# Optimization experiments

Hardware: AMD Instinct MI355X
Metric: run time of the kernel (lower is better)

## Reference

```python
import jax, jax.numpy as jnp
import numpy as np

B, Hdim, Wdim, C, HEADS, WS = 16, 112, 112, 128, 4, 7
VD = C
MLP_H = int(4.0 * VD)
EPS = 1e-5


def _layernorm(x, g, b):
    mu = jnp.mean(x, axis=-1, keepdims=True)
    var = jnp.mean(jnp.square(x - mu), axis=-1, keepdims=True)
    return (x - mu) * jax.lax.rsqrt(var + EPS) * g + b


def _rel_pos_index(ws):
    # static numpy computation, identical to the torch buffer
    coords = np.stack(np.meshgrid(np.arange(ws), np.arange(ws), indexing='ij'))  # (2, ws, ws)
    cf = coords.reshape(2, -1)                       # (2, N)
    rel = cf[:, :, None] - cf[:, None, :]            # (2, N, N)
    rel = rel.transpose(1, 2, 0).copy()              # (N, N, 2)
    rel[:, :, 0] += ws - 1
    rel[:, :, 1] += ws - 1
    rel[:, :, 0] *= 2 * ws - 1
    return jnp.asarray(rel.sum(-1))                  # (N, N) int


def setup_inputs() -> dict:
    key = jax.random.key(0)
    ks = jax.random.split(key, 10)
    nrm = lambda k, s: jax.random.normal(k, s, jnp.float32) * 0.02
    return {
        'x': jax.random.normal(ks[0], (B, Hdim * Wdim, C), jnp.float32),
        'v': jax.random.normal(ks[1], (B, Hdim * Wdim, C), jnp.float32),
        'norm1_g': jnp.ones((C,), jnp.float32), 'norm1_b': jnp.zeros((C,), jnp.float32),
        'normv_g': jnp.ones((C,), jnp.float32), 'normv_b': jnp.zeros((C,), jnp.float32),
        'q_w': nrm(ks[2], (C, C)), 'q_b': jnp.zeros((C,), jnp.float32),
        'kv_w': nrm(ks[3], (2 * C, C)), 'kv_b': jnp.zeros((2 * C,), jnp.float32),
        'rpb_table': nrm(ks[4], ((2 * WS - 1) ** 2, HEADS)),
        'proj_w': nrm(ks[5], (VD, VD)), 'proj_b': jnp.zeros((VD,), jnp.float32),
        'norm2_g': jnp.ones((VD,), jnp.float32), 'norm2_b': jnp.zeros((VD,), jnp.float32),
        'fc1_w': nrm(ks[6], (MLP_H, VD)), 'fc1_b': jnp.zeros((MLP_H,), jnp.float32),
        'fc2_w': nrm(ks[7], (VD, MLP_H)), 'fc2_b': jnp.zeros((VD,), jnp.float32),
        'H': Hdim, 'W': Wdim,
    }


def reference(x, v, norm1_g, norm1_b, normv_g, normv_b, q_w, q_b, kv_w, kv_b,
              rpb_table, proj_w, proj_b, norm2_g, norm2_b, fc1_w, fc1_b,
              fc2_w, fc2_b, H, W):
    Bsz, L, Cd = x.shape
    ws = WS
    heads = HEADS
    hd = Cd // heads
    scale = hd ** (-0.5)

    xs = _layernorm(x, norm1_g, norm1_b).reshape(Bsz, H, W, Cd)
    vs = _layernorm(v, normv_g, normv_b).reshape(Bsz, H, W, Cd)

    pad_b = (ws - H % ws) % ws
    pad_r = (ws - W % ws) % ws
    if pad_b or pad_r:
        xs = jnp.pad(xs, ((0, 0), (0, pad_b), (0, pad_r), (0, 0)))
        vs = jnp.pad(vs, ((0, 0), (0, pad_b), (0, pad_r), (0, 0)))
    Hp, Wp = H + pad_b, W + pad_r

    def part(t):  # window partition -> (nW*B, ws*ws, C)
        return t.reshape(Bsz, Hp // ws, ws, Wp // ws, ws, t.shape[-1]) \
                .transpose(0, 1, 3, 2, 4, 5).reshape(-1, ws * ws, t.shape[-1])

    xw = part(xs)
    vw = part(vs)
    N = ws * ws

    q = (xw @ q_w.T + q_b).reshape(-1, N, heads, hd).transpose(0, 2, 1, 3)   # (B_, h, N, d)
    kv = (vw @ kv_w.T + kv_b).reshape(-1, N, 2, heads, hd).transpose(2, 0, 3, 1, 4)
    k, vv = kv[0], kv[1]

    attn = jnp.einsum('bhnd,bhmd->bhnm', q * scale, k)
    rpi = _rel_pos_index(ws)
    bias = rpb_table[rpi.reshape(-1)].reshape(N, N, heads).transpose(2, 0, 1)  # (h, N, N)
    attn = jax.nn.softmax(attn + bias[None], axis=-1)

    out = jnp.einsum('bhnm,bhmd->bhnd', attn, vv).transpose(0, 2, 1, 3).reshape(-1, N, Cd)
    out = out @ proj_w.T + proj_b

    # window reverse
    out = out.reshape(Bsz, Hp // ws, Wp // ws, ws, ws, VD) \
             .transpose(0, 1, 3, 2, 4, 5).reshape(Bsz, Hp, Wp, VD)
    out = out[:, :H, :W, :].reshape(Bsz, H * W, VD)

    xo = out + x  # residual with pre-norm shortcut
    h = _layernorm(xo, norm2_g, norm2_b)
    h = jax.nn.gelu(h @ fc1_w.T + fc1_b, approximate=False)
    h = h @ fc2_w.T + fc2_b
    return xo + h
```

## Files before the change

kernel.cpp:

```cpp
#include <hip/hip_runtime.h>
#include <hip/hip_bf16.h>
#include <math.h>

typedef __hip_bfloat16 bf16;
typedef __hip_bfloat162 bf162;
typedef __attribute__((ext_vector_type(8))) short bf16x8;
typedef __attribute__((ext_vector_type(4))) short short4v;
typedef __attribute__((ext_vector_type(4))) float f32x4;

__device__ __forceinline__ float b2f(bf16 x){ return __bfloat162float(x); }
__device__ __forceinline__ bf16  f2b(float x){ return __float2bfloat16(x); }
__device__ __forceinline__ short f2bs(float x){ bf16 h = __float2bfloat16(x); return *(short*)&h; }
__device__ __forceinline__ int pack2(float a, float b){
    return ((int)(unsigned short)f2bs(b) << 16) | (int)(unsigned short)f2bs(a);
}

constexpr int kH = 112, kW = 112, kC = 128, kHeads = 4, kWS = 7;
constexpr int kN = 49, kHD = 32, kL = kH * kW;
constexpr int kWinElems = kN * kC;
constexpr int kMLP = 512;
constexpr float kEps = 1e-5f;
constexpr float kScale = 0.17677669529663687f;
constexpr int kAP = 136;

__global__ __launch_bounds__(256) void k_cvt(
    const float* __restrict__ qw, const float* __restrict__ kvw,
    const float* __restrict__ pw, const float* __restrict__ w1,
    const float* __restrict__ w2, short* __restrict__ dst)
{
    const int i = blockIdx.x * 256 + threadIdx.x;
    float val;
    if (i < 16384)       val = qw[i];
    else if (i < 49152)  val = kvw[i - 16384];
    else if (i < 65536)  val = pw[i - 49152];
    else if (i < 131072) val = w1[i - 65536];
    else                 val = w2[i - 131072];
    dst[i] = f2bs(val);
}

__global__ __launch_bounds__(256) void k_ln_qkv_mfma(
    const float* __restrict__ x, const float* __restrict__ v,
    const float* __restrict__ n1g, const float* __restrict__ n1b,
    const float* __restrict__ nvg, const float* __restrict__ nvb,
    const short* __restrict__ qwb, const float* __restrict__ qb,
    const short* __restrict__ kvwb, const float* __restrict__ kvb,
    bf16* __restrict__ qo, bf16* __restrict__ ko, bf16* __restrict__ vo)
{
    __shared__ short Xs[32 * kAP], Vs[32 * kAP];
    const int tid = threadIdx.x, wave = tid >> 6, lane = tid & 63;
    const int quad = lane >> 4, l16 = lane & 15;
    const int row0 = blockIdx.x * 32;
    const int c0 = lane * 2;

    const float g1a = n1g[c0], g1b = n1g[c0 + 1];
    const float b1a = n1b[c0], b1b = n1b[c0 + 1];
    const float gva = nvg[c0], gvb = nvg[c0 + 1];
    const float bva = nvb[c0], bvb = nvb[c0 + 1];
    float2 xv[8], vv[8];
    #pragma unroll
    for (int it = 0; it < 8; it++) {
        const size_t r = (size_t)(row0 + wave + it * 4) * kC;
        xv[it] = *(const float2*)(x + r + c0);
        vv[it] = *(const float2*)(v + r + c0);
    }
    float sx[8], qx[8], sv[8], qv[8];
    #pragma unroll
    for (int it = 0; it < 8; it++) {
        sx[it] = xv[it].x + xv[it].y; qx[it] = xv[it].x * xv[it].x + xv[it].y * xv[it].y;
        sv[it] = vv[it].x + vv[it].y; qv[it] = vv[it].x * vv[it].x + vv[it].y * vv[it].y;
    }
    #pragma unroll
    for (int off = 32; off > 0; off >>= 1) {
        #pragma unroll
        for (int it = 0; it < 8; it++) {
            sx[it] += __shfl_xor(sx[it], off); qx[it] += __shfl_xor(qx[it], off);
            sv[it] += __shfl_xor(sv[it], off); qv[it] += __shfl_xor(qv[it], off);
        }
    }
    #pragma unroll
    for (int it = 0; it < 8; it++) {
        const int n = wave + it * 4;
        const float mux = sx[it] * (1.f / kC);
        const float ivx = rsqrtf(qx[it] * (1.f / kC) - mux * mux + kEps);
        const float muv = sv[it] * (1.f / kC);
        const float ivv = rsqrtf(qv[it] * (1.f / kC) - muv * muv + kEps);
        *(int*)&Xs[n * kAP + c0] = pack2((xv[it].x - mux) * ivx * g1a + b1a,
                                         (xv[it].y - mux) * ivx * g1b + b1b);
        *(int*)&Vs[n * kAP + c0] = pack2((vv[it].x - muv) * ivv * gva + bva,
                                         (vv[it].y - muv) * ivv * gvb + bvb);
    }
    __syncthreads();

    int woff[2];
    #pragma unroll
    for (int mt = 0; mt < 2; mt++) {
        const int gr = row0 + mt * 16 + l16;
        const int b = gr / kL, l = gr - b * kL;
        const int h = l / kW, w_ = l - h * kW;
        woff[mt] = ((b << 8) + (h / 7) * 16 + (w_ / 7)) * kWinElems
                 + ((h % 7) * 7 + (w_ % 7)) * kC;
    }

    bf16x8 xf[2][4], vf[2][4];
    #pragma unroll
    for (int mt = 0; mt < 2; mt++)
        #pragma unroll
        for (int ks = 0; ks < 4; ks++) {
            xf[mt][ks] = *(const bf16x8*)&Xs[(mt * 16 + l16) * kAP + ks * 32 + quad * 8];
            vf[mt][ks] = *(const bf16x8*)&Vs[(mt * 16 + l16) * kAP + ks * 32 + quad * 8];
        }

    auto loadw = [&](bf16x8* dst, int j) {
        const int nt = wave * 6 + j;
        const bool isq = (nt < 8);
        const short* wmat = isq ? qwb : kvwb;
        const int wr0 = (isq ? nt : nt - 8) * 16;
        #pragma unroll
        for (int ks = 0; ks < 4; ks++)
            dst[ks] = *(const bf16x8*)(wmat + (size_t)(wr0 + l16) * kC + ks * 32 + quad * 8);
    };
    bf16x8 wA[4], wB[4];
    loadw(wA, 0);
    #pragma unroll
    for (int j = 0; j < 6; j++) {
        if (j < 5) loadw((j & 1) ? wA : wB, j + 1);
        const bf16x8* wc = (j & 1) ? wB : wA;
        const int nt = wave * 6 + j;
        const bool isq = (nt < 8);
        const float* bias = isq ? qb : kvb;
        const int wr0 = (isq ? nt : nt - 8) * 16;
        const float4 bv4 = *(const float4*)(bias + wr0 + quad * 4);
        f32x4 a0 = { bv4.x, bv4.y, bv4.z, bv4.w };
        f32x4 a1 = a0;
        if (isq) {
            #pragma unroll
            for (int ks = 0; ks < 4; ks++) {
                a0 = __builtin_amdgcn_mfma_f32_16x16x32_bf16(wc[ks], xf[0][ks], a0, 0, 0, 0);
                a1 = __builtin_amdgcn_mfma_f32_16x16x32_bf16(wc[ks], xf[1][ks], a1, 0, 0, 0);
            }
        } else {
            #pragma unroll
            for (int ks = 0; ks < 4; ks++) {
                a0 = __builtin_amdgcn_mfma_f32_16x16x32_bf16(wc[ks], vf[0][ks], a0, 0, 0, 0);
                a1 = __builtin_amdgcn_mfma_f32_16x16x32_bf16(wc[ks], vf[1][ks], a1, 0, 0, 0);
            }
        }
        bf16* dst = isq ? qo : (nt < 16 ? ko : vo);
        const int cb = (isq ? nt : (nt < 16 ? nt - 8 : nt - 16)) * 16 + quad * 4;
        short4v p0, p1;
        #pragma unroll
        for (int i = 0; i < 4; i++) { p0[i] = f2bs(a0[i]); p1[i] = f2bs(a1[i]); }
        *(short4v*)((short*)dst + (size_t)woff[0] + cb) = p0;
        *(short4v*)((short*)dst + (size_t)woff[1] + cb) = p1;
    }
}

__global__ __launch_bounds__(256, 3) void k_attn_mfma(
    bf16* __restrict__ qbuf, const bf16* __restrict__ kbuf,
    const bf16* __restrict__ vbuf, const float* __restrict__ rpb)
{
    __shared__ short Pl[kHeads][64 * 64];
    __shared__ short Vt[kHeads][32 * 64];
    __shared__ float rpl[kHeads][169];
    const int tid = threadIdx.x, wave = tid >> 6, lane = tid & 63;
    const int quad = lane >> 4, l16 = lane & 15;
    const int head = wave;
    const size_t wbase = (size_t)blockIdx.x * kWinElems;

    for (int i = lane; i < 169; i += 64) rpl[head][i] = rpb[i * kHeads + head];

    bf16x8 qf[4], kf[4];
    const bf16* qp = qbuf + wbase + head * kHD + quad * 8;
    const bf16* kp = kbuf + wbase + head * kHD + quad * 8;
    #pragma unroll
    for (int t = 0; t < 4; t++) {
        qf[t] = *(const bf16x8*)(qp + (size_t)(t * 16 + l16) * kC);
        kf[t] = *(const bf16x8*)(kp + (size_t)(t * 16 + l16) * kC);
    }

    #pragma unroll
    for (int h = 0; h < 4; h++) {
        for (int i = tid; i < 1024; i += 256) {
            const int m = i >> 4, d2 = (i & 15) << 1;
            int val = 0;
            if (m < 49) val = *(const int*)(vbuf + wbase + (size_t)m * kC + h * kHD + d2);
            Vt[h][d2 * 64 + (m ^ ((d2 & 7) << 3))]         = (short)(val & 0xffff);
            Vt[h][(d2 + 1) * 64 + (m ^ (((d2 + 1) & 7) << 3))] = (short)(val >> 16);
        }
    }

    f32x4 S[4][4];
    #pragma unroll
    for (int nt = 0; nt < 4; nt++)
        #pragma unroll
        for (int mt = 0; mt < 4; mt++)
            S[nt][mt] = __builtin_amdgcn_mfma_f32_16x16x32_bf16(
                qf[nt], kf[mt], (f32x4){0.f, 0.f, 0.f, 0.f}, 0, 0, 0);

    __syncthreads();

    int an[4][4];
    #pragma unroll
    for (int nt = 0; nt < 4; nt++)
        #pragma unroll
        for (int i = 0; i < 4; i++) {
            const int n = nt * 16 + quad * 4 + i;
            an[nt][i] = 13 * (n / 7) + (n % 7) + 84;
        }
    int bm[4]; bool mok[4];
    #pragma unroll
    for (int mt = 0; mt < 4; mt++) {
        const int m = mt * 16 + l16;
        bm[mt] = 13 * (m / 7) + (m % 7);
        mok[mt] = (m < 49);
    }

    const float* rp = rpl[head];
    #pragma unroll
    for (int nt = 0; nt < 4; nt++)
        #pragma unroll
        for (int i = 0; i < 4; i++) {
            float sv[4];
            #pragma unroll
            for (int mt = 0; mt < 4; mt++) {
                int idx = an[nt][i] - bm[mt];
                idx = ((unsigned)idx > 168u) ? 0 : idx;
                sv[mt] = mok[mt] ? (S[nt][mt][i] * kScale + rp[idx]) : -1e30f;
            }
            float mx = fmaxf(fmaxf(sv[0], sv[1]), fmaxf(sv[2], sv[3]));
            #pragma unroll
            for (int off = 1; off < 16; off <<= 1) mx = fmaxf(mx, __shfl_xor(mx, off));
            float e[4];
            float sum = 0.f;
            #pragma unroll
            for (int mt = 0; mt < 4; mt++) { e[mt] = __expf(sv[mt] - mx); sum += e[mt]; }
            #pragma unroll
            for (int off = 1; off < 16; off <<= 1) sum += __shfl_xor(sum, off);
            const float inv = 1.f / sum;
            const int prow = nt * 16 + quad * 4 + i;
            short* pr = &Pl[head][prow * 64];
            const int sw = (prow & 7) << 3;
            #pragma unroll
            for (int mt = 0; mt < 4; mt++)
                pr[(mt * 16 + l16) ^ sw] = f2bs(e[mt] * inv);
        }

    bf16x8 va[2][2], pb2[4][2];
    #pragma unroll
    for (int dt = 0; dt < 2; dt++)
        #pragma unroll
        for (int ks = 0; ks < 2; ks++) {
            const int r = dt * 16 + l16;
            va[dt][ks] = *(const bf16x8*)&Vt[head][r * 64 + ((ks * 32 + quad * 8) ^ ((r & 7) << 3))];
        }
    #pragma unroll
    for (int nt = 0; nt < 4; nt++)
        #pragma unroll
        for (int ks = 0; ks < 2; ks++) {
            const int r = nt * 16 + l16;
            pb2[nt][ks] = *(const bf16x8*)&Pl[head][r * 64 + ((ks * 32 + quad * 8) ^ ((r & 7) << 3))];
        }
    f32x4 o[2][4];
    #pragma unroll
    for (int dt = 0; dt < 2; dt++)
        #pragma unroll
        for (int nt = 0; nt < 4; nt++) {
            f32x4 a = __builtin_amdgcn_mfma_f32_16x16x32_bf16(
                va[dt][0], pb2[nt][0], (f32x4){0.f, 0.f, 0.f, 0.f}, 0, 0, 0);
            o[dt][nt] = __builtin_amdgcn_mfma_f32_16x16x32_bf16(
                va[dt][1], pb2[nt][1], a, 0, 0, 0);
        }

    #pragma unroll
    for (int nt = 0; nt < 4; nt++) {
        const int n = nt * 16 + l16;
        if (n < 49) {
            bf16* dst = qbuf + wbase + (size_t)n * kC + head * kHD + quad * 4;
            #pragma unroll
            for (int dt = 0; dt < 2; dt++) {
                short4v p;
                #pragma unroll
                for (int i = 0; i < 4; i++) p[i] = f2bs(o[dt][nt][i]);
                *(short4v*)(dst + dt * 16) = p;
            }
        }
    }
}

constexpr int kMT = 32;
constexpr int kAPs = 128;
constexpr int kHPs = 512;

__global__ __launch_bounds__(256, 4) void k_proj_mlp(
    const bf16* __restrict__ ao, const short* __restrict__ pwb,
    const float* __restrict__ pb, const float* __restrict__ x,
    float* __restrict__ out,
    const float* __restrict__ g2, const float* __restrict__ b2v,
    const short* __restrict__ w1b, const float* __restrict__ bb1,
    const short* __restrict__ w2b, const float* __restrict__ bb2)
{
    __shared__ short LDSu[kMT * kAPs + kMT * kHPs];
    short* const A_s = LDSu;
    short* const H_s = LDSu + kMT * kAPs;
    float* const lnscr = (float*)H_s;

    const int tid = threadIdx.x, wave = tid >> 6, lane = tid & 63;
    const int quad = lane >> 4, l16 = lane & 15;
    const size_t row0 = (size_t)blockIdx.x * kMT;
    const int xorm = (l16 & 7) << 3;

    int woff[2];
    #pragma unroll
    for (int mt = 0; mt < 2; mt++) {
        const int gr = (int)row0 + mt * 16 + l16;
        const int b = gr / kL, l = gr - b * kL;
        const int h = l / kW, w_ = l - h * kW;
        woff[mt] = ((b << 8) + (h / 7) * 16 + (w_ / 7)) * kWinElems
                 + ((h % 7) * 7 + (w_ % 7)) * kC;
    }
    bf16x8 bfrag[2][4];
    #pragma unroll
    for (int mt = 0; mt < 2; mt++)
        #pragma unroll
        for (int ks = 0; ks < 4; ks++)
            bfrag[mt][ks] = *(const bf16x8*)((const short*)ao
                                + (size_t)woff[mt] + ks * 32 + quad * 8);

    float4 res[2][2];
    #pragma unroll
    for (int j = 0; j < 2; j++)
        #pragma unroll
        for (int mt = 0; mt < 2; mt++)
            res[j][mt] = *(const float4*)(x + (row0 + mt * 16 + l16) * kC
                                            + (wave * 2 + j) * 16 + quad * 4);
    float4 gv[2], bvv[2];
    #pragma unroll
    for (int j = 0; j < 2; j++) {
        const int cb = (wave * 2 + j) * 16 + quad * 4;
        gv[j]  = *(const float4*)(g2 + cb);
        bvv[j] = *(const float4*)(b2v + cb);
    }

    f32x4 xo[2][2];
    #pragma unroll
    for (int j = 0; j < 2; j++) {
        const int nt = wave * 2 + j;
        const int cb = nt * 16 + quad * 4;
        const float4 pbv = *(const float4*)(pb + cb);
        f32x4 a0 = { pbv.x, pbv.y, pbv.z, pbv.w };
        f32x4 a1 = a0;
        #pragma unroll
        for (int ks = 0; ks < 4; ks++) {
            const bf16x8 af = *(const bf16x8*)(pwb + (size_t)(nt * 16 + l16) * kC + ks * 32 + quad * 8);
            a0 = __builtin_amdgcn_mfma_f32_16x16x32_bf16(af, bfrag[0][ks], a0, 0, 0, 0);
            a1 = __builtin_amdgcn_mfma_f32_16x16x32_bf16(af, bfrag[1][ks], a1, 0, 0, 0);
        }
        #pragma unroll
        for (int i = 0; i < 4; i++) {
            xo[j][0][i] = a0[i] + ((const float*)&res[j][0])[i];
            xo[j][1][i] = a1[i] + ((const float*)&res[j][1])[i];
        }
    }

    float sp[2], qp[2];
    #pragma unroll
    for (int mt = 0; mt < 2; mt++) {
        float s = 0.f, q = 0.f;
        #pragma unroll
        for (int j = 0; j < 2; j++)
            #pragma unroll
            for (int i = 0; i < 4; i++) {
                const float v = xo[j][mt][i];
                s += v; q += v * v;
            }
        s += __shfl_xor(s, 16); q += __shfl_xor(q, 16);
        s += __shfl_xor(s, 32); q += __shfl_xor(q, 32);
        sp[mt] = s; qp[mt] = q;
    }
    if (quad == 0) {
        #pragma unroll
        for (int mt = 0; mt < 2; mt++) {
            float2 pr; pr.x = sp[mt]; pr.y = qp[mt];
            *(float2*)&lnscr[(mt * 16 + l16) * 8 + wave * 2] = pr;
        }
    }
    __syncthreads();

    float mu[2], iv[2];
    #pragma unroll
    for (int mt = 0; mt < 2; mt++) {
        const int r = mt * 16 + l16;
        float s = 0.f, q = 0.f;
        #pragma unroll
        for (int w = 0; w < 4; w++) {
            const float2 pr = *(const float2*)&lnscr[r * 8 + w * 2];
            s += pr.x; q += pr.y;
        }
        mu[mt] = s * (1.f / kC);
        iv[mt] = rsqrtf(q * (1.f / kC) - mu[mt] * mu[mt] + kEps);
    }

    #pragma unroll
    for (int j = 0; j < 2; j++) {
        const int cb = (wave * 2 + j) * 16 + quad * 4;
        #pragma unroll
        for (int mt = 0; mt < 2; mt++) {
            short4v p;
            #pragma unroll
            for (int i = 0; i < 4; i++)
                p[i] = f2bs((xo[j][mt][i] - mu[mt]) * iv[mt]
                            * ((const float*)&gv[j])[i] + ((const float*)&bvv[j])[i]);
            *(short4v*)&A_s[(mt * 16 + l16) * kAPs + (cb ^ xorm)] = p;
        }
    }
    __syncthreads();

    bf16x8 bfrag2[2][4];
    #pragma unroll
    for (int mt = 0; mt < 2; mt++)
        #pragma unroll
        for (int ks = 0; ks < 4; ks++)
            bfrag2[mt][ks] = *(const bf16x8*)&A_s[(mt * 16 + l16) * kAPs
                                + ((ks * 32 + quad * 8) ^ xorm)];

    const short* wbase = w1b + (size_t)(wave * 128 + l16) * kC + quad * 8;
    auto loadw1 = [&](bf16x8* dst, int t) {
        #pragma unroll
        for (int ks = 0; ks < 4; ks++)
            dst[ks] = *(const bf16x8*)(wbase + (size_t)t * (16 * kC) + ks * 32);
    };
    bf16x8 wA[4], wB[4];
    loadw1(wA, 0);
    #pragma unroll
    for (int t = 0; t < 8; t++) {
        if (t < 7) loadw1((t & 1) ? wA : wB, t + 1);
        const bf16x8* wc = (t & 1) ? wB : wA;
        const float4 bi = *(const float4*)(bb1 + (wave * 8 + t) * 16 + quad * 4);
        f32x4 a0 = { bi.x, bi.y, bi.z, bi.w };
        f32x4 a1 = a0;
        #pragma unroll
        for (int ks = 0; ks < 4; ks++) {
            a0 = __builtin_amdgcn_mfma_f32_16x16x32_bf16(wc[ks], bfrag2[0][ks], a0, 0, 0, 0);
            a1 = __builtin_amdgcn_mfma_f32_16x16x32_bf16(wc[ks], bfrag2[1][ks], a1, 0, 0, 0);
        }
        const int nb = (wave * 8 + t) * 16 + quad * 4;
        short4v p0, p1;
        #pragma unroll
        for (int i = 0; i < 4; i++) {
            const float v0 = a0[i], v1 = a1[i];
            p0[i] = f2bs(0.5f * v0 * (1.f + erff(v0 * 0.70710678118f)));
            p1[i] = f2bs(0.5f * v1 * (1.f + erff(v1 * 0.70710678118f)));
        }
        *(short4v*)&H_s[l16 * kHPs + (nb ^ xorm)] = p0;
        *(short4v*)&H_s[(16 + l16) * kHPs + (nb ^ xorm)] = p1;
    }
    __syncthreads();

    const int ct0 = wave * 2;
    f32x4 acc2[2][2];
    #pragma unroll
    for (int t = 0; t < 2; t++) {
        const float4 bi = *(const float4*)(bb2 + (ct0 + t) * 16 + quad * 4);
        acc2[t][0] = (f32x4){ bi.x, bi.y, bi.z, bi.w };
        acc2[t][1] = acc2[t][0];
    }
    const short* w2base = w2b + (size_t)(ct0 * 16 + l16) * kMLP + quad * 8;
    const short* hb0 = &H_s[l16 * kHPs];
    const short* hb1 = &H_s[(16 + l16) * kHPs];
    auto loadh = [&](bf16x8* h, bf16x8* w, int kk) {
        const int col = (kk * 32 + quad * 8) ^ xorm;
        h[0] = *(const bf16x8*)(hb0 + col);
        h[1] = *(const bf16x8*)(hb1 + col);
        w[0] = *(const bf16x8*)(w2base + kk * 32);
        w[1] = *(const bf16x8*)(w2base + (size_t)16 * kMLP + kk * 32);
    };
    auto mfma4 = [&](const bf16x8* h, const bf16x8* w) {
        acc2[0][0] = __builtin_amdgcn_mfma_f32_16x16x32_bf16(w[0], h[0], acc2[0][0], 0, 0, 0);
        acc2[0][1] = __builtin_amdgcn_mfma_f32_16x16x32_bf16(w[0], h[1], acc2[0][1], 0, 0, 0);
        acc2[1][0] = __builtin_amdgcn_mfma_f32_16x16x32_bf16(w[1], h[0], acc2[1][0], 0, 0, 0);
        acc2[1][1] = __builtin_amdgcn_mfma_f32_16x16x32_bf16(w[1], h[1], acc2[1][1], 0, 0, 0);
    };
    bf16x8 hA[2], wwA[2], hB[2], wwB[2];
    loadh(hA, wwA, 0);
    #pragma unroll
    for (int kk = 0; kk < 16; kk += 2) {
        loadh(hB, wwB, kk + 1);
        mfma4(hA, wwA);
        if (kk + 2 < 16) loadh(hA, wwA, kk + 2);
        mfma4(hB, wwB);
    }

    #pragma unroll
    for (int t = 0; t < 2; t++) {
        const int cbv = (ct0 + t) * 16 + quad * 4;
        #pragma unroll
        for (int mt = 0; mt < 2; mt++) {
            const size_t m = row0 + mt * 16 + l16;
            float4 r;
            r.x = xo[t][mt][0] + acc2[t][mt][0];
            r.y = xo[t][mt][1] + acc2[t][mt][1];
            r.z = xo[t][mt][2] + acc2[t][mt][2];
            r.w = xo[t][mt][3] + acc2[t][mt][3];
            *(float4*)(out + m * kC + cbv) = r;
        }
    }
}

extern "C" void kernel_launch(void* const* d_in, const int* in_sizes, int n_in,
                              void* d_out, int out_size, void* d_ws, size_t ws_size,
                              hipStream_t stream) {
    (void)in_sizes; (void)n_in; (void)out_size; (void)ws_size;
    const float* x      = (const float*)d_in[0];
    const float* v      = (const float*)d_in[1];
    const float* n1g    = (const float*)d_in[2];
    const float* n1b    = (const float*)d_in[3];
    const float* nvg    = (const float*)d_in[4];
    const float* nvb    = (const float*)d_in[5];
    const float* q_w    = (const float*)d_in[6];
    const float* q_b    = (const float*)d_in[7];
    const float* kv_w   = (const float*)d_in[8];
    const float* kv_b   = (const float*)d_in[9];
    const float* rpb    = (const float*)d_in[10];
    const float* proj_w = (const float*)d_in[11];
    const float* proj_b = (const float*)d_in[12];
    const float* n2g    = (const float*)d_in[13];
    const float* n2b    = (const float*)d_in[14];
    const float* fc1_w  = (const float*)d_in[15];
    const float* fc1_b  = (const float*)d_in[16];
    const float* fc2_w  = (const float*)d_in[17];
    const float* fc2_b  = (const float*)d_in[18];

    const size_t winTot = (size_t)4096 * kWinElems;
    bf16* qbuf = (bf16*)d_ws;
    bf16* kbuf = qbuf + winTot;
    bf16* vbuf = kbuf + winTot;
    short* wcvt = (short*)(vbuf + winTot);
    short* qwb  = wcvt;
    short* kvwb = qwb + 16384;
    short* pwb  = kvwb + 32768;
    short* w1b  = pwb + 16384;
    short* w2b  = w1b + 65536;
    float* outb = (float*)d_out;

    k_cvt<<<768, 256, 0, stream>>>(q_w, kv_w, proj_w, fc1_w, fc2_w, wcvt);
    k_ln_qkv_mfma<<<6272, 256, 0, stream>>>(x, v, n1g, n1b, nvg, nvb,
                                            qwb, q_b, kvwb, kv_b, qbuf, kbuf, vbuf);
    k_attn_mfma<<<4096, 256, 0, stream>>>(qbuf, kbuf, vbuf, rpb);
    k_proj_mlp<<<6272, 256, 0, stream>>>(qbuf, pwb, proj_b, x, outb,
                                         n2g, n2b, w1b, fc1_b, w2b, fc2_b);
}
```

Measured before the change: 705.1 us.

## Chunk MLP hidden dimension in two halves to halve LDS footprint

Splits the fc1→GELU→fc2 stage into two 256-wide hidden chunks, reusing a half-size LDS buffer for the hidden activations, with extra barriers between chunks. This cuts LDS per block from about 40KB to 24KB so more blocks can be resident per CU. It also moves the first fc1 weight prefetch ahead of the barrier. The cost is an extra synchronisation per block and a less even pipeline between the two GEMMs.

```diff
diff --git a/kernel.cpp b/kernel.cpp
--- a/kernel.cpp
+++ b/kernel.cpp
@@ -289,7 +289,7 @@
 
 constexpr int kMT = 32;
 constexpr int kAPs = 128;
-constexpr int kHPs = 512;
+constexpr int kHC  = 256;
 
 __global__ __launch_bounds__(256, 4) void k_proj_mlp(
     const bf16* __restrict__ ao, const short* __restrict__ pwb,
@@ -299,7 +299,7 @@
     const short* __restrict__ w1b, const float* __restrict__ bb1,
     const short* __restrict__ w2b, const float* __restrict__ bb2)
 {
-    __shared__ short LDSu[kMT * kAPs + kMT * kHPs];
+    __shared__ short LDSu[kMT * kAPs + kMT * kHC];
     short* const A_s = LDSu;
     short* const H_s = LDSu + kMT * kAPs;
     float* const lnscr = (float*)H_s;
@@ -413,6 +413,16 @@
             *(short4v*)&A_s[(mt * 16 + l16) * kAPs + (cb ^ xorm)] = p;
         }
     }
+
+    auto loadw1 = [&](bf16x8* dst, int u) {
+        const int ntg = (u >> 2) * 16 + wave * 4 + (u & 3);
+        const short* p = w1b + (size_t)(ntg * 16 + l16) * kC + quad * 8;
+        #pragma unroll
+        for (int ks = 0; ks < 4; ks++)
+            dst[ks] = *(const bf16x8*)(p + ks * 32);
+    };
+    bf16x8 wA[4], wB[4];
+    loadw1(wA, 0);
     __syncthreads();
 
     bf16x8 bfrag2[2][4];
@@ -422,39 +432,6 @@
         for (int ks = 0; ks < 4; ks++)
             bfrag2[mt][ks] = *(const bf16x8*)&A_s[(mt * 16 + l16) * kAPs
                                 + ((ks * 32 + quad * 8) ^ xorm)];
-
-    const short* wbase = w1b + (size_t)(wave * 128 + l16) * kC + quad * 8;
-    auto loadw1 = [&](bf16x8* dst, int t) {
-        #pragma unroll
-        for (int ks = 0; ks < 4; ks++)
-            dst[ks] = *(const bf16x8*)(wbase + (size_t)t * (16 * kC) + ks * 32);
-    };
-    bf16x8 wA[4], wB[4];
-    loadw1(wA, 0);
-    #pragma unroll
-    for (int t = 0; t < 8; t++) {
-        if (t < 7) loadw1((t & 1) ? wA : wB, t + 1);
-        const bf16x8* wc = (t & 1) ? wB : wA;
-        const float4 bi = *(const float4*)(bb1 + (wave * 8 + t) * 16 + quad * 4);
-        f32x4 a0 = { bi.x, bi.y, bi.z, bi.w };
-        f32x4 a1 = a0;
-        #pragma unroll
-        for (int ks = 0; ks < 4; ks++) {
-            a0 = __builtin_amdgcn_mfma_f32_16x16x32_bf16(wc[ks], bfrag2[0][ks], a0, 0, 0, 0);
-            a1 = __builtin_amdgcn_mfma_f32_16x16x32_bf16(wc[ks], bfrag2[1][ks], a1, 0, 0, 0);
-        }
-        const int nb = (wave * 8 + t) * 16 + quad * 4;
-        short4v p0, p1;
-        #pragma unroll
-        for (int i = 0; i < 4; i++) {
-            const float v0 = a0[i], v1 = a1[i];
-            p0[i] = f2bs(0.5f * v0 * (1.f + erff(v0 * 0.70710678118f)));
-            p1[i] = f2bs(0.5f * v1 * (1.f + erff(v1 * 0.70710678118f)));
-        }
-        *(short4v*)&H_s[l16 * kHPs + (nb ^ xorm)] = p0;
-        *(short4v*)&H_s[(16 + l16) * kHPs + (nb ^ xorm)] = p1;
-    }
-    __syncthreads();
 
     const int ct0 = wave * 2;
     f32x4 acc2[2][2];
@@ -465,14 +442,18 @@
         acc2[t][1] = acc2[t][0];
     }
     const short* w2base = w2b + (size_t)(ct0 * 16 + l16) * kMLP + quad * 8;
-    const short* hb0 = &H_s[l16 * kHPs];
-    const short* hb1 = &H_s[(16 + l16) * kHPs];
-    auto loadh = [&](bf16x8* h, bf16x8* w, int kk) {
+    const short* hb0 = &H_s[l16 * kHC];
+    const short* hb1 = &H_s[(16 + l16) * kHC];
+    bf16x8 hA[2], wwA[2], hB[2], wwB[2];
+    auto loadw2 = [&](bf16x8* w, int c, int kk) {
+        const int col = c * 256 + kk * 32;
+        w[0] = *(const bf16x8*)(w2base + col);
+        w[1] = *(const bf16x8*)(w2base + (size_t)16 * kMLP + col);
+    };
+    auto loadhh = [&](bf16x8* h, int kk) {
         const int col = (kk * 32 + quad * 8) ^ xorm;
         h[0] = *(const bf16x8*)(hb0 + col);
         h[1] = *(const bf16x8*)(hb1 + col);
-        w[0] = *(const bf16x8*)(w2base + kk * 32);
-        w[1] = *(const bf16x8*)(w2base + (size_t)16 * kMLP + kk * 32);
     };
     auto mfma4 = [&](const bf16x8* h, const bf16x8* w) {
         acc2[0][0] = __builtin_amdgcn_mfma_f32_16x16x32_bf16(w[0], h[0], acc2[0][0], 0, 0, 0);
@@ -480,14 +461,45 @@
         acc2[1][0] = __builtin_amdgcn_mfma_f32_16x16x32_bf16(w[1], h[0], acc2[1][0], 0, 0, 0);
         acc2[1][1] = __builtin_amdgcn_mfma_f32_16x16x32_bf16(w[1], h[1], acc2[1][1], 0, 0, 0);
     };
-    bf16x8 hA[2], wwA[2], hB[2], wwB[2];
-    loadh(hA, wwA, 0);
-    #pragma unroll
-    for (int kk = 0; kk < 16; kk += 2) {
-        loadh(hB, wwB, kk + 1);
-        mfma4(hA, wwA);
-        if (kk + 2 < 16) loadh(hA, wwA, kk + 2);
-        mfma4(hB, wwB);
+
+    #pragma unroll
+    for (int c = 0; c < 2; c++) {
+        if (c) __syncthreads();
+        #pragma unroll
+        for (int t = 0; t < 4; t++) {
+            const int u = c * 4 + t;
+            if (u < 7) loadw1(((u + 1) & 1) ? wB : wA, u + 1);
+            const bf16x8* wc = (u & 1) ? wB : wA;
+            const int ntg = (u >> 2) * 16 + wave * 4 + (u & 3);
+            const float4 bi = *(const float4*)(bb1 + ntg * 16 + quad * 4);
+            f32x4 a0 = { bi.x, bi.y, bi.z, bi.w };
+            f32x4 a1 = a0;
+            #pragma unroll
+            for (int ks = 0; ks < 4; ks++) {
+                a0 = __builtin_amdgcn_mfma_f32_16x16x32_bf16(wc[ks], bfrag2[0][ks], a0, 0, 0, 0);
+                a1 = __builtin_amdgcn_mfma_f32_16x16x32_bf16(wc[ks], bfrag2[1][ks], a1, 0, 0, 0);
+            }
+            const int nb = (wave * 4 + t) * 16 + quad * 4;
+            short4v p0, p1;
+            #pragma unroll
+            for (int i = 0; i < 4; i++) {
+                const float v0 = a0[i], v1 = a1[i];
+                p0[i] = f2bs(0.5f * v0 * (1.f + erff(v0 * 0.70710678118f)));
+                p1[i] = f2bs(0.5f * v1 * (1.f + erff(v1 * 0.70710678118f)));
+            }
+            *(short4v*)&H_s[l16 * kHC + (nb ^ xorm)] = p0;
+            *(short4v*)&H_s[(16 + l16) * kHC + (nb ^ xorm)] = p1;
+        }
+        loadw2(wwA, c, 0);
+        __syncthreads();
+        loadhh(hA, 0);
+        #pragma unroll
+        for (int kk = 0; kk < 8; kk += 2) {
+            loadw2(wwB, c, kk + 1); loadhh(hB, kk + 1);
+            mfma4(hA, wwA);
+            if (kk + 2 < 8) { loadw2(wwA, c, kk + 2); loadhh(hA, kk + 2); }
+            mfma4(hB, wwB);
+        }
     }
 
     #pragma unroll
```

Result: no change. 711.3 us (+0.9%).
